# Kernel optimization log

Measured on AMD Instinct MI355X. Metric: run time of the kernel, lower is better.

The kernel has to match this reference:

```python
import jax, jax.numpy as jnp
import numpy as np

WAY = 5
EPS = 1e-12  # torch F.normalize eps


def setup_inputs() -> dict:
    key = jax.random.key(0)
    k1, k2, k3, k4 = jax.random.split(key, 4)
    n_support, n_queries = 25, 200
    f_g, f_l, d = 16, 64, 512
    return {
        "support_set_global": jax.random.normal(k1, (n_support, f_g, d), jnp.float32),
        "support_set_local": jax.random.normal(k2, (n_support, f_l, d), jnp.float32),
        "support_labels": (jnp.arange(n_support) % WAY).astype(jnp.int64),
        "queries_global": jax.random.normal(k3, (n_queries, f_g, d), jnp.float32),
        "queries_local": jax.random.normal(k4, (n_queries, f_l, d), jnp.float32),
    }


def _l2norm(x):
    # torch F.normalize(dim=1) with eps clamp
    n = jnp.linalg.norm(x, axis=-1, keepdims=True)
    return x / jnp.maximum(n, EPS)


def reference(support_set_global, support_set_local, support_labels,
              queries_global, queries_local):
    # Dropout is identity in eval mode; omitted for a deterministic reference.
    S = jnp.concatenate([support_set_global, support_set_local], axis=1)  # [nS, F, D]
    Q = jnp.concatenate([queries_global, queries_local], axis=1)          # [nQ, F, D]
    nS, F, D = S.shape
    nQ = Q.shape[0]

    Sn = _l2norm(S.reshape(nS * F, D))
    Qn = _l2norm(Q.reshape(nQ * F, D))

    # cosine-sim matmul: [nS*F, nQ*F]
    sim = Sn @ Qn.T
    # view(nS, F, nQ, F).transpose(2,1) -> [nS, nQ, F, F]
    sim = sim.reshape(nS, F, nQ, F).transpose(0, 2, 1, 3)
    dmat = 1.0 - sim

    # squared Frobenius norm over last two dims, keepdim -> [nS, nQ, 1, 1]
    fro2 = jnp.sum(dmat * dmat, axis=(-2, -1))  # [nS, nQ]
    # dists.min(3)[0].sum(2) + dists.min(2)[0].sum(2) over singleton dims == 2 * fro2
    cum_dists = 2.0 * fro2  # [nS, nQ]

    # per-class mean over support rows (class-wise gather-mean)
    counts = jax.ops.segment_sum(jnp.ones((nS,), cum_dists.dtype), support_labels,
                                 num_segments=WAY)                       # [WAY]
    class_sum = jax.ops.segment_sum(cum_dists, support_labels, num_segments=WAY)  # [WAY, nQ]
    class_dists = class_sum / counts[:, None]

    logits = -class_dists.T  # [nQ, WAY]
    return logits
```

## Files before the change

kernel.cpp:

```cpp
#include <hip/hip_runtime.h>

#define NS 25
#define NQ 200
#define FG 16
#define FL 64
#define FTOT 80
#define D 512
#define WAY 5
#define MROWS 2000
#define MPAD 2080
#define NROWS 16000

typedef unsigned char u8;
typedef __attribute__((ext_vector_type(4))) float floatx4;
typedef __attribute__((ext_vector_type(4))) int intx4;
typedef __attribute__((ext_vector_type(8))) int intx8;

__device__ inline void gload_lds16(const void* g, void* l) {
    __builtin_amdgcn_global_load_lds(
        (const __attribute__((address_space(1))) unsigned int*)g,
        (__attribute__((address_space(3))) unsigned int*)l, 16, 0, 0);
}

__global__ void normalize_kernel(const float* __restrict__ sg, const float* __restrict__ sl,
                                 const float* __restrict__ qg, const float* __restrict__ ql,
                                 u8* __restrict__ Sn, u8* __restrict__ Qn,
                                 const int* __restrict__ labels,
                                 float* __restrict__ out, float* __restrict__ rcnt) {
    if (blockIdx.x == 4500) {
        intx4 z = {0, 0, 0, 0};
        intx4* pad = (intx4*)(Sn + (size_t)MROWS * D);
        for (int i = threadIdx.x; i < (MPAD - MROWS) * D / 16; i += 256) pad[i] = z;
        for (int i = threadIdx.x; i < NQ * WAY; i += 256) out[i] = 0.f;
        if (threadIdx.x == 0) {
            int counts[WAY] = {0, 0, 0, 0, 0};
            for (int s = 0; s < NS; ++s) counts[labels[s]]++;
            for (int c = 0; c < WAY; ++c) rcnt[c] = 1.0f / (float)(counts[c] ? counts[c] : 1);
        }
        return;
    }
    int wave = (blockIdx.x * blockDim.x + threadIdx.x) >> 6;
    int lane = threadIdx.x & 63;
    const int totalRows = MROWS + NROWS;
    if (wave >= totalRows) return;

    const float* src;
    u8* dst;
    if (wave < MROWS) {
        int s = wave / FTOT, f = wave % FTOT;
        src = (f < FG) ? sg + (size_t)(s * FG + f) * D
                       : sl + (size_t)(s * FL + (f - FG)) * D;
        dst = Sn + (size_t)wave * D;
    } else {
        int r = wave - MROWS;
        int q = r / FTOT, f = r % FTOT;
        src = (f < FG) ? qg + (size_t)(q * FG + f) * D
                       : ql + (size_t)(q * FL + (f - FG)) * D;
        dst = Qn + (size_t)r * D;
    }

    float4 v0 = ((const float4*)src)[2 * lane];
    float4 v1 = ((const float4*)src)[2 * lane + 1];
    float ss = v0.x*v0.x + v0.y*v0.y + v0.z*v0.z + v0.w*v0.w
             + v1.x*v1.x + v1.y*v1.y + v1.z*v1.z + v1.w*v1.w;
    #pragma unroll
    for (int off = 32; off > 0; off >>= 1) ss += __shfl_xor(ss, off, 64);
    float scale = 1.0f / fmaxf(sqrtf(ss), 1e-12f);

    int w0 = __builtin_amdgcn_cvt_pk_fp8_f32(v0.x * scale, v0.y * scale, 0, false);
    w0     = __builtin_amdgcn_cvt_pk_fp8_f32(v0.z * scale, v0.w * scale, w0, true);
    int w1 = __builtin_amdgcn_cvt_pk_fp8_f32(v1.x * scale, v1.y * scale, 0, false);
    w1     = __builtin_amdgcn_cvt_pk_fp8_f32(v1.z * scale, v1.w * scale, w1, true);
    ((int2*)dst)[lane] = make_int2(w0, w1);
}

__global__ __launch_bounds__(256, 3) void gemm_kernel(const u8* __restrict__ Sn,
                                                      const u8* __restrict__ Qn,
                                                      const int* __restrict__ labels,
                                                      const float* __restrict__ rcnt,
                                                      float* __restrict__ out) {
    __shared__ u8 As[160][128];
    __shared__ u8 Bs[160][128];

    const int bx = blockIdx.x;
    const int by = blockIdx.y;
    const int tid = threadIdx.x;
    const int lane = tid & 63;
    const int w = tid >> 6;
    const int lm = lane & 15;
    const int lq = lane >> 4;
    const int wr = w >> 1;
    const int wc = w & 1;

    floatx4 acc[5][5];
    #pragma unroll
    for (int i = 0; i < 5; ++i)
        #pragma unroll
        for (int j = 0; j < 5; ++j) acc[i][j] = (floatx4){0.f, 0.f, 0.f, 0.f};

    const u8* Sbase = Sn + (size_t)by * 160 * D;
    const u8* Qbase = Qn + (size_t)bx * 160 * D;

    const u8* gsrc = (w < 2) ? Sbase : Qbase;
    u8* ldst = (w < 2) ? (u8*)As : (u8*)Bs;
    const int sl0 = (w & 1) * 10;
    const int grow = lane >> 3;
    const int gc = lane & 7;

    #pragma unroll 1
    for (int kc = 0; kc < 4; ++kc) {
        const int k0 = kc * 128;
        __syncthreads();
        #pragma unroll
        for (int t = 0; t < 10; ++t) {
            const int sl = sl0 + t;
            const int r = sl * 8 + grow;
            const int cp = gc ^ ((r >> 1) & 7);
            gload_lds16(gsrc + (size_t)r * D + k0 + cp * 16, ldst + sl * 1024);
        }
        __syncthreads();

        intx8 bfr[5];
        #pragma unroll
        for (int j = 0; j < 5; ++j) {
            const int r = wc * 80 + j * 16 + lm;
            const int s = (r >> 1) & 7;
            intx4 lo = *(const intx4*)(&Bs[r][((2 * lq + 0) ^ s) * 16]);
            intx4 hi = *(const intx4*)(&Bs[r][((2 * lq + 1) ^ s) * 16]);
            bfr[j][0] = lo[0]; bfr[j][1] = lo[1]; bfr[j][2] = lo[2]; bfr[j][3] = lo[3];
            bfr[j][4] = hi[0]; bfr[j][5] = hi[1]; bfr[j][6] = hi[2]; bfr[j][7] = hi[3];
        }
        #pragma unroll
        for (int i = 0; i < 5; ++i) {
            const int r = wr * 80 + i * 16 + lm;
            const int s = (r >> 1) & 7;
            intx4 lo = *(const intx4*)(&As[r][((2 * lq + 0) ^ s) * 16]);
            intx4 hi = *(const intx4*)(&As[r][((2 * lq + 1) ^ s) * 16]);
            intx8 afr;
            afr[0] = lo[0]; afr[1] = lo[1]; afr[2] = lo[2]; afr[3] = lo[3];
            afr[4] = hi[0]; afr[5] = hi[1]; afr[6] = hi[2]; afr[7] = hi[3];
            #pragma unroll
            for (int j = 0; j < 5; ++j)
                acc[i][j] = __builtin_amdgcn_mfma_scale_f32_16x16x128_f8f6f4(
                    afr, bfr[j], acc[i][j], 0, 0,
                    0, 0x7F7F7F7F, 0, 0x7F7F7F7F);
        }
    }

    float local = 0.f;
    #pragma unroll
    for (int i = 0; i < 5; ++i)
        #pragma unroll
        for (int j = 0; j < 5; ++j)
            #pragma unroll
            for (int r = 0; r < 4; ++r) {
                const float d = 1.0f - acc[i][j][r];
                local = fmaf(d, d, local);
            }
    #pragma unroll
    for (int off = 32; off > 0; off >>= 1) local += __shfl_down(local, off, 64);

    const int sIdx = by * 2 + wr;
    const int qIdx = bx * 2 + wc;
    if (lane == 0 && sIdx < NS) {
        const int c = labels[sIdx];
        atomicAdd(&out[qIdx * WAY + c], -2.0f * local * rcnt[c]);
    }
}

extern "C" void kernel_launch(void* const* d_in, const int* in_sizes, int n_in,
                              void* d_out, int out_size, void* d_ws, size_t ws_size,
                              hipStream_t stream) {
    const float* sg = (const float*)d_in[0];
    const float* sl = (const float*)d_in[1];
    const int* labels = (const int*)d_in[2];
    const float* qg = (const float*)d_in[3];
    const float* ql = (const float*)d_in[4];
    float* out = (float*)d_out;

    u8* Sn = (u8*)d_ws;
    u8* Qn = Sn + (size_t)MPAD * D;
    float* rcnt = (float*)(Qn + (size_t)NROWS * D);

    normalize_kernel<<<4501, 256, 0, stream>>>(sg, sl, qg, ql, Sn, Qn, labels, out, rcnt);
    dim3 g2(100, 13);
    gemm_kernel<<<g2, 256, 0, stream>>>(Sn, Qn, labels, rcnt, out);
}
```

Baseline: 124.1 us.

## Double-buffer Q tiles in LDS and load S fragments directly into registers

The GEMM kernel now keeps two LDS buffers for the query tile and prefetches the next K chunk while the MFMAs for the current chunk run, so the loop needs one barrier per iteration instead of two. The support-side A fragments are no longer staged through LDS; each wave reads them straight from global memory into registers, and the next chunk's fragments are loaded after the current MFMAs. Launch bounds drop from 3 to 2 blocks per SM to leave room for the extra registers. The goal is to hide global load latency behind compute, at the cost of lower occupancy and duplicated global reads of S rows by the two waves that share them.

New measurement: 121.6 us. 1.02x faster.

```diff
diff --git a/kernel.cpp b/kernel.cpp
--- a/kernel.cpp
+++ b/kernel.cpp
@@ -74,13 +74,12 @@
     ((int2*)dst)[lane] = make_int2(w0, w1);
 }
 
-__global__ __launch_bounds__(256, 3) void gemm_kernel(const u8* __restrict__ Sn,
+__global__ __launch_bounds__(256, 2) void gemm_kernel(const u8* __restrict__ Sn,
                                                       const u8* __restrict__ Qn,
                                                       const int* __restrict__ labels,
                                                       const float* __restrict__ rcnt,
                                                       float* __restrict__ out) {
-    __shared__ u8 As[160][128];
-    __shared__ u8 Bs[160][128];
+    __shared__ __align__(16) u8 Bs[2][160][128];
 
     const int bx = blockIdx.x;
     const int by = blockIdx.y;
@@ -98,53 +97,73 @@
         #pragma unroll
         for (int j = 0; j < 5; ++j) acc[i][j] = (floatx4){0.f, 0.f, 0.f, 0.f};
 
-    const u8* Sbase = Sn + (size_t)by * 160 * D;
+    const u8* Abase = Sn + (size_t)(by * 160 + wr * 80 + lm) * D + lq * 32;
     const u8* Qbase = Qn + (size_t)bx * 160 * D;
-
-    const u8* gsrc = (w < 2) ? Sbase : Qbase;
-    u8* ldst = (w < 2) ? (u8*)As : (u8*)Bs;
-    const int sl0 = (w & 1) * 10;
+    u8* BsFlat = &Bs[0][0][0];
+
     const int grow = lane >> 3;
     const int gc = lane & 7;
-
-    #pragma unroll 1
+    const int sl0 = w * 5;
+
+    #pragma unroll
+    for (int t = 0; t < 5; ++t) {
+        const int sl = sl0 + t;
+        const int r = sl * 8 + grow;
+        const int cp = gc ^ ((r >> 1) & 7);
+        gload_lds16(Qbase + (size_t)r * D + cp * 16, BsFlat + sl * 1024);
+    }
+    intx8 afr[5];
+    #pragma unroll
+    for (int i = 0; i < 5; ++i) {
+        intx4 lo = *(const intx4*)(Abase + i * 16 * D);
+        intx4 hi = *(const intx4*)(Abase + i * 16 * D + 16);
+        afr[i][0] = lo[0]; afr[i][1] = lo[1]; afr[i][2] = lo[2]; afr[i][3] = lo[3];
+        afr[i][4] = hi[0]; afr[i][5] = hi[1]; afr[i][6] = hi[2]; afr[i][7] = hi[3];
+    }
+    __syncthreads();
+
+    #pragma unroll
     for (int kc = 0; kc < 4; ++kc) {
-        const int k0 = kc * 128;
-        __syncthreads();
-        #pragma unroll
-        for (int t = 0; t < 10; ++t) {
-            const int sl = sl0 + t;
-            const int r = sl * 8 + grow;
-            const int cp = gc ^ ((r >> 1) & 7);
-            gload_lds16(gsrc + (size_t)r * D + k0 + cp * 16, ldst + sl * 1024);
-        }
-        __syncthreads();
-
+        if (kc < 3) {
+            const int k0 = (kc + 1) * 128;
+            u8* dstb = BsFlat + ((kc + 1) & 1) * 20480;
+            #pragma unroll
+            for (int t = 0; t < 5; ++t) {
+                const int sl = sl0 + t;
+                const int r = sl * 8 + grow;
+                const int cp = gc ^ ((r >> 1) & 7);
+                gload_lds16(Qbase + (size_t)r * D + k0 + cp * 16, dstb + sl * 1024);
+            }
+        }
+        const u8* curb = BsFlat + (kc & 1) * 20480;
         intx8 bfr[5];
         #pragma unroll
         for (int j = 0; j < 5; ++j) {
             const int r = wc * 80 + j * 16 + lm;
             const int s = (r >> 1) & 7;
-            intx4 lo = *(const intx4*)(&Bs[r][((2 * lq + 0) ^ s) * 16]);
-            intx4 hi = *(const intx4*)(&Bs[r][((2 * lq + 1) ^ s) * 16]);
+            intx4 lo = *(const intx4*)(curb + r * 128 + ((2 * lq + 0) ^ s) * 16);
+            intx4 hi = *(const intx4*)(curb + r * 128 + ((2 * lq + 1) ^ s) * 16);
             bfr[j][0] = lo[0]; bfr[j][1] = lo[1]; bfr[j][2] = lo[2]; bfr[j][3] = lo[3];
             bfr[j][4] = hi[0]; bfr[j][5] = hi[1]; bfr[j][6] = hi[2]; bfr[j][7] = hi[3];
         }
         #pragma unroll
-        for (int i = 0; i < 5; ++i) {
-            const int r = wr * 80 + i * 16 + lm;
-            const int s = (r >> 1) & 7;
-            intx4 lo = *(const intx4*)(&As[r][((2 * lq + 0) ^ s) * 16]);
-            intx4 hi = *(const intx4*)(&As[r][((2 * lq + 1) ^ s) * 16]);
-            intx8 afr;
-            afr[0] = lo[0]; afr[1] = lo[1]; afr[2] = lo[2]; afr[3] = lo[3];
-            afr[4] = hi[0]; afr[5] = hi[1]; afr[6] = hi[2]; afr[7] = hi[3];
+        for (int i = 0; i < 5; ++i)
             #pragma unroll
             for (int j = 0; j < 5; ++j)
                 acc[i][j] = __builtin_amdgcn_mfma_scale_f32_16x16x128_f8f6f4(
-                    afr, bfr[j], acc[i][j], 0, 0,
+                    afr[i], bfr[j], acc[i][j], 0, 0,
                     0, 0x7F7F7F7F, 0, 0x7F7F7F7F);
-        }
+        if (kc < 3) {
+            const int k0 = (kc + 1) * 128;
+            #pragma unroll
+            for (int i = 0; i < 5; ++i) {
+                intx4 lo = *(const intx4*)(Abase + i * 16 * D + k0);
+                intx4 hi = *(const intx4*)(Abase + i * 16 * D + k0 + 16);
+                afr[i][0] = lo[0]; afr[i][1] = lo[1]; afr[i][2] = lo[2]; afr[i][3] = lo[3];
+                afr[i][4] = hi[0]; afr[i][5] = hi[1]; afr[i][6] = hi[2]; afr[i][7] = hi[3];
+            }
+        }
+        __syncthreads();
     }
 
     float local = 0.f;
```
